# Performance work log

Hardware: AMD Instinct MI355X
Metric: run time of the kernel (lower is better)

The kernel has to match this reference:

```python
import jax, jax.numpy as jnp
import numpy as np

N, M, E, F = 100000, 20000, 1000000, 128
LEAKY_SLOPE = 0.2
BN_EPS = 1e-5


def segment_softmax(logits, seg, num_segments):
    # numerically stable softmax over ragged segments
    mx = jax.ops.segment_max(logits, seg, num_segments=num_segments)
    mx = jnp.where(jnp.isfinite(mx), mx, 0.0)  # empty segments -> -inf -> 0
    e = jnp.exp(logits - mx[seg])
    s = jax.ops.segment_sum(e, seg, num_segments=num_segments)
    return e / (s[seg] + 1e-16)


def setup_inputs() -> dict:
    key = jax.random.key(0)
    ks = jax.random.split(key, 6)
    return {
        "x": jax.random.normal(ks[0], (N, F), jnp.float32),
        "hyperedge_attr": jax.random.normal(ks[1], (M, F), jnp.float32),
        "W": jax.random.normal(ks[2], (F, F), jnp.float32) / np.sqrt(F),
        "att": jax.random.normal(ks[3], (2 * F,), jnp.float32) * 0.1,
        "bias": jnp.zeros((F,), jnp.float32),
        "gamma": jnp.ones((F,), jnp.float32),
        "beta": jnp.zeros((F,), jnp.float32),
        "node_idx": jax.random.randint(ks[4], (E,), 0, N, dtype=jnp.int32),
        "edge_idx": jax.random.randint(ks[5], (E,), 0, M, dtype=jnp.int32),
    }


def reference(x, hyperedge_attr, W, att, bias, gamma, beta, node_idx, edge_idx):
    # --- HypergraphConv(use_attention=True, heads=1, attention_mode='node') ---
    xw = x @ W                     # [N, F] transformed node features
    ea = hyperedge_attr @ W        # [M, F] transformed hyperedge features (shared lin)

    # per-incidence attention logits: (cat[x_i, e_j] * att).sum(-1)
    a_node = xw @ att[:F]          # [N]
    a_edge = ea @ att[F:]          # [M]
    alpha = a_node[node_idx] + a_edge[edge_idx]          # [E]
    alpha = jax.nn.leaky_relu(alpha, LEAKY_SLOPE)
    alpha = segment_softmax(alpha, edge_idx, M)          # softmax per hyperedge

    ones = jnp.ones((E,), xw.dtype)
    D = jax.ops.segment_sum(ones, node_idx, num_segments=N)   # node degree
    Dinv = jnp.where(D > 0, 1.0 / D, 0.0)
    Bdeg = jax.ops.segment_sum(ones, edge_idx, num_segments=M)  # hyperedge size
    Binv = jnp.where(Bdeg > 0, 1.0 / Bdeg, 0.0)

    # node -> hyperedge: gather node feats, weight by B^{-1}*alpha, scatter to edges
    m1 = (Binv[edge_idx] * alpha)[:, None] * xw[node_idx]        # [E, F]
    edge_feat = jax.ops.segment_sum(m1, edge_idx, num_segments=M)  # [M, F]

    # hyperedge -> node: gather edge feats, weight by D^{-1}*alpha, scatter to nodes
    m2 = (Dinv[node_idx] * alpha)[:, None] * edge_feat[edge_idx]  # [E, F]
    out = jax.ops.segment_sum(m2, node_idx, num_segments=N) + bias  # [N, F]

    # --- BatchNorm1d (training-mode batch statistics, biased variance) ---
    mu = out.mean(axis=0)
    var = out.var(axis=0)
    out = gamma * (out - mu) * jax.lax.rsqrt(var + BN_EPS) + beta

    # --- ELU, dropout (eval: identity), residual (in_dim == out_dim) ---
    out = jax.nn.elu(out)
    return out + x
```

## Files before the change

### kernel.cpp

```cpp
#include <hip/hip_runtime.h>
#include <hip/hip_bf16.h>

#define NN 100000
#define MM 20000
#define EE 1000000
#define FF 128

#define EBK 157
#define NBK 782
#define ECAP 7168
#define NCAP 1664
#define CHUNK 2048
#define NREP 64
#define BM 32
#define GEMM_BLOCKS (NN / BM)
#define AEDGE_BLOCKS (MM / 4)
#define BINA_BLOCKS ((EE + CHUNK - 1) / CHUNK)
#define SMEM_BYTES 8448

typedef unsigned short u16;
typedef unsigned int u32;
typedef __attribute__((ext_vector_type(8))) short short8v;
typedef __attribute__((ext_vector_type(4))) float f32x4;

__device__ __forceinline__ u16 f2bf(float f) {
  u32 x = __float_as_uint(f);
  return (u16)((x + 0x7FFFu + ((x >> 16) & 1u)) >> 16);
}
__device__ __forceinline__ float bf2f(u16 u) { return __uint_as_float(((u32)u) << 16); }
__device__ __forceinline__ float leaky(float v) { return v > 0.f ? v : 0.2f * v; }
__device__ __forceinline__ float readlane_f(float v, int l) {
  return __uint_as_float((u32)__builtin_amdgcn_readlane((int)__float_as_uint(v), l));
}

__global__ __launch_bounds__(256) void k_prep(const float* __restrict__ W,
                                              const float* __restrict__ att,
                                              float* __restrict__ watt2, u16* __restrict__ WtSwz,
                                              int* __restrict__ ecur, int* __restrict__ ncur,
                                              float* __restrict__ bn_partial) {
  int gid = blockIdx.x * 256 + threadIdx.x;
  if (gid < EBK) ecur[gid] = 0;
  if (gid < NBK) ncur[gid] = 0;
  if (gid < NREP * 256) bn_partial[gid] = 0.f;
  if (blockIdx.x == 0 && threadIdx.x < 128) {
    int t = threadIdx.x;
    float s2 = 0.f;
    for (int c = 0; c < FF; c += 4) {
      float4 wv = *(const float4*)(W + t * FF + c);
      s2 += wv.x * att[FF + c] + wv.y * att[FF + c + 1] + wv.z * att[FF + c + 2] + wv.w * att[FF + c + 3];
    }
    watt2[t] = s2;
    int c = t;
    for (int k = 0; k < FF; k += 2) {
      u32 p = (u32)f2bf(W[k * FF + c]) | ((u32)f2bf(W[(k + 1) * FF + c]) << 16);
      int byte = c * 256 + ((k * 2) ^ ((c & 7) << 4));
      *(u32*)((char*)WtSwz + byte) = p;
    }
  }
}

__global__ __launch_bounds__(256) void k_mega(const float* __restrict__ x,
                                              const u16* __restrict__ WtSwz,
                                              const float* __restrict__ att,
                                              u16* __restrict__ xw,
                                              float* __restrict__ a_node,
                                              const float* __restrict__ he,
                                              const float* __restrict__ watt2,
                                              float* __restrict__ a_edge,
                                              const int* __restrict__ node_idx,
                                              const int* __restrict__ edge_idx,
                                              int* __restrict__ ecur, int* __restrict__ ncur,
                                              u32* __restrict__ ebins, u32* __restrict__ nbins) {
  __shared__ char smem[SMEM_BYTES];
  int t = threadIdx.x;
  int bid = blockIdx.x;

  if (bid < BINA_BLOCKS) {
    int* ecnt = (int*)smem;
    int* ncnt = ecnt + EBK;
    int* ebase = ncnt + NBK;
    int* nbase = ebase + EBK;
    for (int i = t; i < EBK; i += 256) ecnt[i] = 0;
    for (int i = t; i < NBK; i += 256) ncnt[i] = 0;
    __syncthreads();
    int start = bid * CHUNK;
    int end = min(start + CHUNK, EE);
    for (int e = start + t; e < end; e += 256) {
      int m = edge_idx[e], n = node_idx[e];
      atomicAdd(&ecnt[m >> 7], 1);
      atomicAdd(&ncnt[n >> 7], 1);
    }
    __syncthreads();
    for (int i = t; i < EBK; i += 256) {
      int c = ecnt[i];
      ebase[i] = c ? atomicAdd(&ecur[i], c) : 0;
      ecnt[i] = 0;
    }
    for (int i = t; i < NBK; i += 256) {
      int c = ncnt[i];
      nbase[i] = c ? atomicAdd(&ncur[i], c) : 0;
      ncnt[i] = 0;
    }
    __syncthreads();
    for (int e = start + t; e < end; e += 256) {
      int m = edge_idx[e], n = node_idx[e];
      int eb = m >> 7, nb = n >> 7;
      int p = ebase[eb] + atomicAdd(&ecnt[eb], 1);
      if (p < ECAP) ebins[(size_t)eb * ECAP + p] = ((u32)n << 7) | (u32)(m & 127);
      int q = nbase[nb] + atomicAdd(&ncnt[nb], 1);
      if (q < NCAP) nbins[(size_t)nb * NCAP + q] = ((u32)m << 7) | (u32)(n & 127);
    }
    return;
  }

  if (bid >= BINA_BLOCKS + GEMM_BLOCKS) {
    int m = ((bid - BINA_BLOCKS - GEMM_BLOCKS) * 256 + t) >> 6;
    int lane = t & 63;
    float2 wv = ((const float2*)watt2)[lane];
    float2 v = ((const float2*)(he + (size_t)m * FF))[lane];
    float p = v.x * wv.x + v.y * wv.y;
#pragma unroll
    for (int off = 32; off; off >>= 1) p += __shfl_xor(p, off, 64);
    if (lane == 0) a_edge[m] = p;
    return;
  }

  u16* xl = (u16*)smem;
  float* pn = (float*)(smem + 8192);
  if (t < BM) pn[t] = 0.f;
  int row0 = (bid - BINA_BLOCKS) * BM;
  for (int chunk = t; chunk < BM * 32; chunk += 256) {
    int r = chunk >> 5;
    int j = chunk & 31;
    float4 v = ((const float4*)(x + (size_t)(row0 + r) * FF))[j];
    uint2 p;
    p.x = (u32)f2bf(v.x) | ((u32)f2bf(v.y) << 16);
    p.y = (u32)f2bf(v.z) | ((u32)f2bf(v.w) << 16);
    int byte = r * 256 + ((j * 8) ^ ((r & 7) << 4));
    *(uint2*)((char*)xl + byte) = p;
  }
  __syncthreads();

  int wid = t >> 6, lane = t & 63;
  int rt = wid & 1, ch = wid >> 1;
  int r_lo = lane & 15, khalf = lane >> 4;
  f32x4 acc[4];
#pragma unroll
  for (int ct = 0; ct < 4; ++ct) acc[ct] = (f32x4){0.f, 0.f, 0.f, 0.f};

#pragma unroll
  for (int kc = 0; kc < 4; ++kc) {
    int kbyte = kc * 64 + khalf * 16;
    int arow = rt * 16 + r_lo;
    short8v a = *(const short8v*)((const char*)xl + arow * 256 + (kbyte ^ ((arow & 7) << 4)));
#pragma unroll
    for (int ct = 0; ct < 4; ++ct) {
      int brow = ch * 64 + ct * 16 + r_lo;
      short8v b = *(const short8v*)((const char*)WtSwz + brow * 256 + (kbyte ^ ((brow & 7) << 4)));
      acc[ct] = __builtin_amdgcn_mfma_f32_16x16x32_bf16(a, b, acc[ct], 0, 0, 0);
    }
  }

  float att_c[4];
#pragma unroll
  for (int ct = 0; ct < 4; ++ct) att_c[ct] = att[ch * 64 + ct * 16 + r_lo];
  float p[4] = {0.f, 0.f, 0.f, 0.f};
#pragma unroll
  for (int ct = 0; ct < 4; ++ct) {
#pragma unroll
    for (int reg = 0; reg < 4; ++reg) {
      int lrow = rt * 16 + khalf * 4 + reg;
      xw[(size_t)(row0 + lrow) * FF + ch * 64 + ct * 16 + r_lo] = f2bf(acc[ct][reg]);
      p[reg] += acc[ct][reg] * att_c[ct];
    }
  }
#pragma unroll
  for (int off = 1; off <= 8; off <<= 1) {
#pragma unroll
    for (int reg = 0; reg < 4; ++reg) p[reg] += __shfl_xor(p[reg], off, 64);
  }
  if (r_lo == 0) {
#pragma unroll
    for (int reg = 0; reg < 4; ++reg)
      atomicAdd(&pn[rt * 16 + khalf * 4 + reg], p[reg]);
  }
  __syncthreads();
  if (t < BM) a_node[row0 + t] = pn[t];
}

__global__ __launch_bounds__(256) void k_binB(const u32* __restrict__ ebins,
                                              const int* __restrict__ ecur,
                                              int* __restrict__ edge_ptr,
                                              uint2* __restrict__ pairE,
                                              const u32* __restrict__ nbins,
                                              const int* __restrict__ ncur,
                                              int* __restrict__ node_ptr,
                                              uint2* __restrict__ pairN,
                                              const float* __restrict__ a_node,
                                              const float* __restrict__ a_edge) {
  __shared__ int cnt[128], cur[128], sc[128];
  __shared__ int ps[256];
  __shared__ float loc[128];
  int t = threadIdx.x;
  bool is_edge = blockIdx.x < EBK;
  int b = is_edge ? blockIdx.x : blockIdx.x - EBK;
  const int* curArr = is_edge ? ecur : ncur;
  const u32* src = is_edge ? (ebins + (size_t)b * ECAP) : (nbins + (size_t)b * NCAP);
  int count = is_edge ? min(ecur[b], ECAP) : min(ncur[b], NCAP);
  int* ptr = is_edge ? edge_ptr : node_ptr;
  uint2* pairArr = is_edge ? pairE : pairN;
  const float* gatherA = is_edge ? a_node : a_edge;
  int glen = is_edge ? MM : NN;
  int nbk = is_edge ? EBK : NBK;

  if (t < 128) {
    int g = b * 128 + t;
    loc[t] = (g < glen) ? (is_edge ? a_edge[g] : a_node[g]) : 0.f;
  }

  int acc = 0;
  for (int i = t; i < b; i += 256) acc += curArr[i];
  ps[t] = acc;
  __syncthreads();
  for (int off = 128; off; off >>= 1) {
    if (t < off) ps[t] += ps[t + off];
    __syncthreads();
  }
  int gbase = ps[0];

  if (t < 128) cnt[t] = 0;
  __syncthreads();
  for (int i = t; i < count; i += 256) atomicAdd(&cnt[src[i] & 127], 1);
  __syncthreads();
  if (t < 128) sc[t] = cnt[t];
  __syncthreads();
  for (int off = 1; off < 128; off <<= 1) {
    int u = (t >= off && t < 128) ? sc[t - off] : 0;
    __syncthreads();
    if (t < 128) sc[t] += u;
    __syncthreads();
  }
  if (t < 128) {
    int excl = sc[t] - cnt[t];
    cur[t] = excl;
    int g = b * 128 + t;
    if (g < glen) ptr[g] = gbase + excl;
  }
  if (b == nbk - 1 && t == 0) ptr[glen] = gbase + count;
  __syncthreads();
  for (int i = t; i < count; i += 256) {
    u32 v = src[i];
    int lo = v & 127;
    int other = (int)(v >> 7);
    int pos = atomicAdd(&cur[lo], 1);
    float uw = __expf(leaky(gatherA[other] + loc[lo]));
    pairArr[gbase + pos] = make_uint2((u32)other, __float_as_uint(uw));
  }
}

__global__ __launch_bounds__(256) void k_edge_agg(const int* __restrict__ edge_ptr,
                                                  const uint2* __restrict__ pairE,
                                                  const u16* __restrict__ xw,
                                                  u16* __restrict__ edge_feat) {
  int wid = threadIdx.x >> 6, lane = threadIdx.x & 63;
  int m = blockIdx.x * 4 + wid;
  int pv_l = (lane < 5) ? edge_ptr[blockIdx.x * 4 + lane] : 0;
  int s0 = __builtin_amdgcn_readlane(pv_l, wid);
  int s1 = __builtin_amdgcn_readlane(pv_l, wid + 1);
  int len = s1 - s0;
  if (len == 0) return;

  float ssum_l = 0.f;
  float accx = 0.f, accy = 0.f;
  for (int base = s0; base < s1; base += 64) {
    int i = base + lane;
    bool valid = i < s1;
    uint2 pv = valid ? pairE[i] : make_uint2(0u, 0u);
    int n_l = (int)pv.x;
    float w_l = __uint_as_float(pv.y);
    ssum_l += w_l;
    int cnt = min(64, s1 - base);
    for (int b = 0; b < cnt; b += 16) {
      u32 u[16];
      float wv[16];
#pragma unroll
      for (int j = 0; j < 16; ++j) {
        int n = __builtin_amdgcn_readlane(n_l, b + j);
        wv[j] = readlane_f(w_l, b + j);
        u[j] = *(const u32*)(xw + (size_t)n * FF + 2 * lane);
      }
#pragma unroll
      for (int j = 0; j < 16; ++j) {
        accx += wv[j] * bf2f((u16)u[j]);
        accy += wv[j] * bf2f((u16)(u[j] >> 16));
      }
    }
  }
#pragma unroll
  for (int off = 1; off < 64; off <<= 1) ssum_l += __shfl_xor(ssum_l, off, 64);
  float invs = 1.0f / (ssum_l + 1e-16f);
  float r = invs * invs / (float)len;
  u32 packed = (u32)f2bf(accx * r) | ((u32)f2bf(accy * r) << 16);
  *(u32*)(edge_feat + (size_t)m * FF + 2 * lane) = packed;
}

__global__ __launch_bounds__(256) void k_node_agg(const int* __restrict__ node_ptr,
                                                  const uint2* __restrict__ pairN,
                                                  const u16* __restrict__ edge_feat,
                                                  const float* __restrict__ bias,
                                                  float* __restrict__ out_f32,
                                                  u16* __restrict__ raw_bf,
                                                  float* __restrict__ bn_partial) {
  __shared__ float4 sd[4][64];
  int wid = threadIdx.x >> 6, lane = threadIdx.x & 63;
  float2 bv = ((const float2*)bias)[lane];
  int n0 = blockIdx.x * 16 + wid * 4;
  int pv_l = (lane < 5) ? node_ptr[n0 + lane] : 0;
  float s1x = 0.f, s1y = 0.f, s2x = 0.f, s2y = 0.f;
#pragma unroll
  for (int k = 0; k < 4; ++k) {
    int n = n0 + k;
    int s0 = __builtin_amdgcn_readlane(pv_l, k);
    int s1 = __builtin_amdgcn_readlane(pv_l, k + 1);
    float accx = 0.f, accy = 0.f;
    for (int base = s0; base < s1; base += 64) {
      int i = base + lane;
      bool valid = i < s1;
      uint2 pv = valid ? pairN[i] : make_uint2(0u, 0u);
      int m_l = (int)pv.x;
      float w_l = __uint_as_float(pv.y);
      int cnt = min(64, s1 - base);
      for (int b = 0; b < cnt; b += 16) {
        u32 u[16];
        float wv[16];
#pragma unroll
        for (int j = 0; j < 16; ++j) {
          int mm = __builtin_amdgcn_readlane(m_l, b + j);
          wv[j] = readlane_f(w_l, b + j);
          u[j] = *(const u32*)(edge_feat + (size_t)mm * FF + 2 * lane);
        }
#pragma unroll
        for (int j = 0; j < 16; ++j) {
          accx += wv[j] * bf2f((u16)u[j]);
          accy += wv[j] * bf2f((u16)(u[j] >> 16));
        }
      }
    }
    int deg = s1 - s0;
    float dinv = deg > 0 ? 1.0f / (float)deg : 0.f;
    float ox = accx * dinv + bv.x;
    float oy = accy * dinv + bv.y;
    if (raw_bf) {
      *(u32*)(raw_bf + (size_t)n * FF + 2 * lane) = (u32)f2bf(ox) | ((u32)f2bf(oy) << 16);
    } else {
      ((float2*)(out_f32 + (size_t)n * FF))[lane] = make_float2(ox, oy);
    }
    s1x += ox; s1y += oy;
    s2x += ox * ox; s2y += oy * oy;
  }
  sd[wid][lane] = make_float4(s1x, s1y, s2x, s2y);
  __syncthreads();
  if (wid == 0) {
    float4 a0 = sd[0][lane], a1 = sd[1][lane], a2 = sd[2][lane], a3 = sd[3][lane];
    float4 s;
    s.x = a0.x + a1.x + a2.x + a3.x;
    s.y = a0.y + a1.y + a2.y + a3.y;
    s.z = a0.z + a1.z + a2.z + a3.z;
    s.w = a0.w + a1.w + a2.w + a3.w;
    float* bp = bn_partial + (blockIdx.x & (NREP - 1)) * 256;
    atomicAdd(bp + 2 * lane, s.x);
    atomicAdd(bp + 2 * lane + 1, s.y);
    atomicAdd(bp + 128 + 2 * lane, s.z);
    atomicAdd(bp + 128 + 2 * lane + 1, s.w);
  }
}

__global__ void k_bn_final(const float* __restrict__ bn_partial, const float* __restrict__ gamma,
                           const float* __restrict__ beta, float* __restrict__ ss) {
  int c = threadIdx.x;
  float s1 = 0.f, s2 = 0.f;
  for (int r = 0; r < NREP; ++r) {
    s1 += bn_partial[r * 256 + c];
    s2 += bn_partial[r * 256 + 128 + c];
  }
  float mu = s1 * (1.0f / NN);
  float var = s2 * (1.0f / NN) - mu * mu;
  var = fmaxf(var, 0.f);
  float sc = gamma[c] * rsqrtf(var + 1e-5f);
  ss[c] = sc;
  ss[FF + c] = beta[c] - mu * sc;
}

__global__ __launch_bounds__(256) void k_finalize(float* __restrict__ out,
                                                  const u16* __restrict__ raw_bf,
                                                  const float* __restrict__ x,
                                                  const float* __restrict__ ss) {
  int idx = blockIdx.x * 256 + threadIdx.x;
  float4 v;
  if (raw_bf) {
    ushort4 rv = *(const ushort4*)(raw_bf + (size_t)idx * 4);
    v = make_float4(bf2f(rv.x), bf2f(rv.y), bf2f(rv.z), bf2f(rv.w));
  } else {
    v = ((const float4*)out)[idx];
  }
  float4 xr = ((const float4*)x)[idx];
  int cb = (idx * 4) & 127;
  float4 sc = *(const float4*)(ss + cb);
  float4 sh = *(const float4*)(ss + FF + cb);
  v.x = fmaf(v.x, sc.x, sh.x);
  v.y = fmaf(v.y, sc.y, sh.y);
  v.z = fmaf(v.z, sc.z, sh.z);
  v.w = fmaf(v.w, sc.w, sh.w);
  v.x = v.x > 0.f ? v.x : expm1f(v.x);
  v.y = v.y > 0.f ? v.y : expm1f(v.y);
  v.z = v.z > 0.f ? v.z : expm1f(v.z);
  v.w = v.w > 0.f ? v.w : expm1f(v.w);
  v.x += xr.x; v.y += xr.y; v.z += xr.z; v.w += xr.w;
  ((float4*)out)[idx] = v;
}

extern "C" void kernel_launch(void* const* d_in, const int* in_sizes, int n_in,
                              void* d_out, int out_size, void* d_ws, size_t ws_size,
                              hipStream_t stream) {
  const float* x     = (const float*)d_in[0];
  const float* he    = (const float*)d_in[1];
  const float* W     = (const float*)d_in[2];
  const float* att   = (const float*)d_in[3];
  const float* bias  = (const float*)d_in[4];
  const float* gamma = (const float*)d_in[5];
  const float* beta  = (const float*)d_in[6];
  const int* node_idx = (const int*)d_in[7];
  const int* edge_idx = (const int*)d_in[8];
  float* out = (float*)d_out;

  char* w = (char*)d_ws;
  auto alloc = [&](size_t bytes) -> char* {
    char* p = w;
    w += (bytes + 255) & ~(size_t)255;
    return p;
  };
  u16*   xw        = (u16*)  alloc((size_t)NN * FF * 2);
  float* a_node    = (float*)alloc((size_t)NN * 4);
  float* a_edge    = (float*)alloc((size_t)MM * 4);
  u16*   WtSwz     = (u16*)  alloc((size_t)FF * FF * 2);
  float* watt2     = (float*)alloc(FF * 4);
  u16*   edge_feat = (u16*)  alloc((size_t)MM * FF * 2);
  int* edge_ptr    = (int*)  alloc((size_t)(MM + 1) * 4);
  int* node_ptr    = (int*)  alloc((size_t)(NN + 1) * 4);
  uint2* pairE     = (uint2*)alloc((size_t)EE * 8);
  uint2* pairN     = (uint2*)alloc((size_t)EE * 8);
  int* ecur        = (int*)  alloc((size_t)EBK * 4);
  int* ncur        = (int*)  alloc((size_t)NBK * 4);
  u32* ebins       = (u32*)  alloc((size_t)EBK * ECAP * 4);
  u32* nbins       = (u32*)  alloc((size_t)NBK * NCAP * 4);
  float* bn_partial= (float*)alloc((size_t)NREP * 256 * 4);
  float* ss        = (float*)alloc(2 * FF * 4);
  u16*   raw_cand  = (u16*)  alloc((size_t)NN * FF * 2);
  size_t need = (size_t)(w - (char*)d_ws);
  u16* raw_bf = (need <= ws_size) ? raw_cand : (u16*)nullptr;

  k_prep<<<64, 256, 0, stream>>>(W, att, watt2, WtSwz, ecur, ncur, bn_partial);
  k_mega<<<BINA_BLOCKS + GEMM_BLOCKS + AEDGE_BLOCKS, 256, 0, stream>>>(
      x, WtSwz, att, xw, a_node, he, watt2, a_edge,
      node_idx, edge_idx, ecur, ncur, ebins, nbins);

  k_binB<<<EBK + NBK, 256, 0, stream>>>(ebins, ecur, edge_ptr, pairE,
                                        nbins, ncur, node_ptr, pairN,
                                        a_node, a_edge);

  k_edge_agg<<<MM / 4, 256, 0, stream>>>(edge_ptr, pairE, xw, edge_feat);
  k_node_agg<<<NN / 16, 256, 0, stream>>>(node_ptr, pairN, edge_feat, bias, out, raw_bf, bn_partial);
  k_bn_final<<<1, 128, 0, stream>>>(bn_partial, gamma, beta, ss);
  k_finalize<<<(NN * FF / 4 + 255) / 256, 256, 0, stream>>>(out, raw_bf, x, ss);
}
```

Baseline: 189.8 us.

## Replicate bin cursors eightfold to cut global atomic contention in binning

Splits each coarse bin's global cursor into 8 replicas selected by block id, with separate capacity slots per replica, so fewer blocks contend on the same atomic counter. The binning pass also switches to 256 larger chunks, which lowers the number of global atomics per bin. The consumer kernel now sums the replica counts for its prefix and loops over the replica segments. A tradeoff is that the smaller per-replica capacities (1024 and 256) could overflow on skewed inputs and silently drop entries, and the prefix loop now reads 8 times as many counters.

```diff
diff --git a/kernel.cpp b/kernel.cpp
--- a/kernel.cpp
+++ b/kernel.cpp
@@ -8,14 +8,15 @@
 
 #define EBK 157
 #define NBK 782
-#define ECAP 7168
-#define NCAP 1664
-#define CHUNK 2048
+#define NREPL 8
+#define ECAPR 1024
+#define NCAPR 256
+#define CHUNK 3907
 #define NREP 64
 #define BM 32
 #define GEMM_BLOCKS (NN / BM)
 #define AEDGE_BLOCKS (MM / 4)
-#define BINA_BLOCKS ((EE + CHUNK - 1) / CHUNK)
+#define BINA_BLOCKS 256
 #define SMEM_BYTES 8448
 
 typedef unsigned short u16;
@@ -39,8 +40,8 @@
                                               int* __restrict__ ecur, int* __restrict__ ncur,
                                               float* __restrict__ bn_partial) {
   int gid = blockIdx.x * 256 + threadIdx.x;
-  if (gid < EBK) ecur[gid] = 0;
-  if (gid < NBK) ncur[gid] = 0;
+  if (gid < NREPL * EBK) ecur[gid] = 0;
+  if (gid < NREPL * NBK) ncur[gid] = 0;
   if (gid < NREP * 256) bn_partial[gid] = 0.f;
   if (blockIdx.x == 0 && threadIdx.x < 128) {
     int t = threadIdx.x;
@@ -80,6 +81,7 @@
     int* ncnt = ecnt + EBK;
     int* ebase = ncnt + NBK;
     int* nbase = ebase + EBK;
+    int rep = bid & (NREPL - 1);
     for (int i = t; i < EBK; i += 256) ecnt[i] = 0;
     for (int i = t; i < NBK; i += 256) ncnt[i] = 0;
     __syncthreads();
@@ -93,12 +95,12 @@
     __syncthreads();
     for (int i = t; i < EBK; i += 256) {
       int c = ecnt[i];
-      ebase[i] = c ? atomicAdd(&ecur[i], c) : 0;
+      ebase[i] = c ? atomicAdd(&ecur[rep * EBK + i], c) : 0;
       ecnt[i] = 0;
     }
     for (int i = t; i < NBK; i += 256) {
       int c = ncnt[i];
-      nbase[i] = c ? atomicAdd(&ncur[i], c) : 0;
+      nbase[i] = c ? atomicAdd(&ncur[rep * NBK + i], c) : 0;
       ncnt[i] = 0;
     }
     __syncthreads();
@@ -106,9 +108,11 @@
       int m = edge_idx[e], n = node_idx[e];
       int eb = m >> 7, nb = n >> 7;
       int p = ebase[eb] + atomicAdd(&ecnt[eb], 1);
-      if (p < ECAP) ebins[(size_t)eb * ECAP + p] = ((u32)n << 7) | (u32)(m & 127);
+      if (p < ECAPR)
+        ebins[(size_t)eb * (NREPL * ECAPR) + rep * ECAPR + p] = ((u32)n << 7) | (u32)(m & 127);
       int q = nbase[nb] + atomicAdd(&ncnt[nb], 1);
-      if (q < NCAP) nbins[(size_t)nb * NCAP + q] = ((u32)m << 7) | (u32)(n & 127);
+      if (q < NCAPR)
+        nbins[(size_t)nb * (NREPL * NCAPR) + rep * NCAPR + q] = ((u32)m << 7) | (u32)(n & 127);
     }
     return;
   }
@@ -201,25 +205,33 @@
   __shared__ int cnt[128], cur[128], sc[128];
   __shared__ int ps[256];
   __shared__ float loc[128];
+  __shared__ int rcnt[NREPL];
   int t = threadIdx.x;
   bool is_edge = blockIdx.x < EBK;
   int b = is_edge ? blockIdx.x : blockIdx.x - EBK;
   const int* curArr = is_edge ? ecur : ncur;
-  const u32* src = is_edge ? (ebins + (size_t)b * ECAP) : (nbins + (size_t)b * NCAP);
-  int count = is_edge ? min(ecur[b], ECAP) : min(ncur[b], NCAP);
+  int BK = is_edge ? EBK : NBK;
+  int CAPR = is_edge ? ECAPR : NCAPR;
+  const u32* binsBase = is_edge ? ebins : nbins;
   int* ptr = is_edge ? edge_ptr : node_ptr;
   uint2* pairArr = is_edge ? pairE : pairN;
   const float* gatherA = is_edge ? a_node : a_edge;
   int glen = is_edge ? MM : NN;
   int nbk = is_edge ? EBK : NBK;
 
+  if (t < NREPL) rcnt[t] = min(curArr[t * BK + b], CAPR);
   if (t < 128) {
     int g = b * 128 + t;
     loc[t] = (g < glen) ? (is_edge ? a_edge[g] : a_node[g]) : 0.f;
   }
 
   int acc = 0;
-  for (int i = t; i < b; i += 256) acc += curArr[i];
+  for (int i = t; i < b; i += 256) {
+    int s = 0;
+#pragma unroll
+    for (int r = 0; r < NREPL; ++r) s += min(curArr[r * BK + i], CAPR);
+    acc += s;
+  }
   ps[t] = acc;
   __syncthreads();
   for (int off = 128; off; off >>= 1) {
@@ -227,10 +239,17 @@
     __syncthreads();
   }
   int gbase = ps[0];
+  int count = 0;
+#pragma unroll
+  for (int r = 0; r < NREPL; ++r) count += rcnt[r];
 
   if (t < 128) cnt[t] = 0;
   __syncthreads();
-  for (int i = t; i < count; i += 256) atomicAdd(&cnt[src[i] & 127], 1);
+  for (int r = 0; r < NREPL; ++r) {
+    const u32* src = binsBase + (size_t)b * (NREPL * CAPR) + r * CAPR;
+    int c = rcnt[r];
+    for (int i = t; i < c; i += 256) atomicAdd(&cnt[src[i] & 127], 1);
+  }
   __syncthreads();
   if (t < 128) sc[t] = cnt[t];
   __syncthreads();
@@ -248,13 +267,17 @@
   }
   if (b == nbk - 1 && t == 0) ptr[glen] = gbase + count;
   __syncthreads();
-  for (int i = t; i < count; i += 256) {
-    u32 v = src[i];
-    int lo = v & 127;
-    int other = (int)(v >> 7);
-    int pos = atomicAdd(&cur[lo], 1);
-    float uw = __expf(leaky(gatherA[other] + loc[lo]));
-    pairArr[gbase + pos] = make_uint2((u32)other, __float_as_uint(uw));
+  for (int r = 0; r < NREPL; ++r) {
+    const u32* src = binsBase + (size_t)b * (NREPL * CAPR) + r * CAPR;
+    int c = rcnt[r];
+    for (int i = t; i < c; i += 256) {
+      u32 v = src[i];
+      int lo = v & 127;
+      int other = (int)(v >> 7);
+      int pos = atomicAdd(&cur[lo], 1);
+      float uw = __expf(leaky(gatherA[other] + loc[lo]));
+      pairArr[gbase + pos] = make_uint2((u32)other, __float_as_uint(uw));
+    }
   }
 }
 
@@ -449,10 +472,10 @@
   int* node_ptr    = (int*)  alloc((size_t)(NN + 1) * 4);
   uint2* pairE     = (uint2*)alloc((size_t)EE * 8);
   uint2* pairN     = (uint2*)alloc((size_t)EE * 8);
-  int* ecur        = (int*)  alloc((size_t)EBK * 4);
-  int* ncur        = (int*)  alloc((size_t)NBK * 4);
-  u32* ebins       = (u32*)  alloc((size_t)EBK * ECAP * 4);
-  u32* nbins       = (u32*)  alloc((size_t)NBK * NCAP * 4);
+  int* ecur        = (int*)  alloc((size_t)NREPL * EBK * 4);
+  int* ncur        = (int*)  alloc((size_t)NREPL * NBK * 4);
+  u32* ebins       = (u32*)  alloc((size_t)EBK * NREPL * ECAPR * 4);
+  u32* nbins       = (u32*)  alloc((size_t)NBK * NREPL * NCAPR * 4);
   float* bn_partial= (float*)alloc((size_t)NREP * 256 * 4);
   float* ss        = (float*)alloc(2 * FF * 4);
   u16*   raw_cand  = (u16*)  alloc((size_t)NN * FF * 2);
```

Result: faster. 172.3 us, median of 2 (-9.2%).
